# Optimization experiments

Measured on AMD Instinct MI355X. Metric: run time of the kernel, lower is better.

The kernel has to match this reference:

```python
import jax, jax.numpy as jnp
import numpy as np

B, L, D = 2, 2048, 1024
H, HD = 16, 64
MAX_LEN = 4096


def rotate_half(t):
    t1, t2 = jnp.split(t, 2, axis=-1)
    return jnp.concatenate([-t2, t1], axis=-1)


def setup_inputs() -> dict:
    key = jax.random.key(0)
    ks = jax.random.split(key, 6)
    # rope tables computed the standard way (cos/sin of position*inv_freq)
    inv_freq = 1.0 / (10000.0 ** (np.arange(0, HD, 2, dtype=np.float32) / HD))
    pos = np.arange(MAX_LEN, dtype=np.float32)
    freqs = np.einsum('l,f->lf', pos, inv_freq)          # [MAX_LEN, HD/2]
    emb = np.concatenate([freqs, freqs], axis=-1)        # [MAX_LEN, HD]
    return {
        'x': jax.random.normal(ks[0], (B, L, D), dtype=jnp.float32),
        'rope_cos': jnp.asarray(np.cos(emb)),
        'rope_sin': jnp.asarray(np.sin(emb)),
        'W_qkv': jax.random.normal(ks[1], (D, 3 * H * HD), dtype=jnp.float32) * (D ** -0.5),
        'W_out': jax.random.normal(ks[2], (H * HD, D), dtype=jnp.float32) * ((H * HD) ** -0.5),
        'b_out': jnp.zeros((D,), dtype=jnp.float32),
    }


def reference(x, rope_cos, rope_sin, W_qkv, W_out, b_out):
    Bb, Ll, Dd = x.shape
    qkv = jnp.einsum('bld,de->ble', x, W_qkv)            # fused QKV projection
    q, k, v = jnp.split(qkv, 3, axis=-1)
    # [B, h, L, d]
    q = q.reshape(Bb, Ll, H, HD).transpose(0, 2, 1, 3)
    k = k.reshape(Bb, Ll, H, HD).transpose(0, 2, 1, 3)
    v = v.reshape(Bb, Ll, H, HD).transpose(0, 2, 1, 3)
    cos = rope_cos[:Ll][None, None, :, :]                # [1,1,L,d]
    sin = rope_sin[:Ll][None, None, :, :]
    q = q * cos + rotate_half(q) * sin
    k = k * cos + rotate_half(k) * sin
    # causal scaled dot-product attention
    scale = HD ** -0.5
    scores = jnp.einsum('bhqd,bhkd->bhqk', q, k) * scale
    causal = jnp.tril(jnp.ones((Ll, Ll), dtype=bool))
    scores = jnp.where(causal[None, None], scores, jnp.finfo(scores.dtype).min)
    attn = jax.nn.softmax(scores, axis=-1)
    out = jnp.einsum('bhqk,bhkd->bhqd', attn, v)
    out = out.transpose(0, 2, 1, 3).reshape(Bb, Ll, H * HD)
    return jnp.einsum('ble,ed->bld', out, W_out) + b_out
```

## Files before the change

### kernel.cpp

```cpp
#include <hip/hip_runtime.h>
#include <math.h>

#define BQ 2
#define LQ 2048
#define DQ 1024
#define HQ 16
#define HDQ 64

typedef __bf16 bf16_t;
typedef bf16_t bf16x4 __attribute__((ext_vector_type(4)));
typedef bf16_t bf16x8 __attribute__((ext_vector_type(8)));
typedef _Float16 f16_t;
typedef f16_t f16x4 __attribute__((ext_vector_type(4)));
typedef f16_t f16x8 __attribute__((ext_vector_type(8)));
typedef float f32x4 __attribute__((ext_vector_type(4)));

__global__ __launch_bounds__(256) void prep_kernel(
    const float* __restrict__ x, const float* __restrict__ Wqkv,
    const float* __restrict__ Wout, const float* __restrict__ cosT,
    const float* __restrict__ sinT,
    bf16_t* __restrict__ xb, bf16_t* __restrict__ Wqkvt,
    bf16_t* __restrict__ Wot, float4* __restrict__ rpk)
{
    __shared__ float t[32][33];
    const int bid = blockIdx.x, tid = threadIdx.x;
    if (bid < 4096) {
        const int i = (bid * 256 + tid) * 4;
        float4 v = *(const float4*)(x + i);
        bf16x4 o;
        o[0] = (bf16_t)v.x; o[1] = (bf16_t)v.y; o[2] = (bf16_t)v.z; o[3] = (bf16_t)v.w;
        *(bf16x4*)(xb + i) = o;
    } else if (bid < 8192) {
        const bool isq = bid < 7168;
        const int b = isq ? bid - 4096 : bid - 7168;
        const int N = isq ? 3072 : 1024;
        const int gx = isq ? 96 : 32;
        const float* in = isq ? Wqkv : Wout;
        bf16_t* out = isq ? Wqkvt : Wot;
        const int k0 = (b / gx) * 32, n0 = (b % gx) * 32;
        const int r = tid >> 3, c4 = (tid & 7) * 4;
        float4 v = *(const float4*)(in + (size_t)(k0 + r) * N + n0 + c4);
        t[r][c4 + 0] = v.x; t[r][c4 + 1] = v.y;
        t[r][c4 + 2] = v.z; t[r][c4 + 3] = v.w;
        __syncthreads();
        bf16x4 o;
        o[0] = (bf16_t)t[c4 + 0][r]; o[1] = (bf16_t)t[c4 + 1][r];
        o[2] = (bf16_t)t[c4 + 2][r]; o[3] = (bf16_t)t[c4 + 3][r];
        *(bf16x4*)(out + (size_t)(n0 + r) * 1024 + k0 + c4) = o;
    } else {
        const int idx = (bid - 8192) * 256 + tid;
        const int i = idx & 15, l = idx >> 4;
        rpk[idx] = make_float4(cosT[l * 64 + i], cosT[l * 64 + 16 + i],
                               sinT[l * 64 + i], sinT[l * 64 + 16 + i]);
    }
}

__global__ __launch_bounds__(256) void qkv_gemm_kernel(
    const bf16_t* __restrict__ A, const bf16_t* __restrict__ Bt,
    bf16_t* __restrict__ qo, bf16_t* __restrict__ ko, f16_t* __restrict__ vo,
    const float4* __restrict__ rpk)
{
    __shared__ __align__(16) bf16_t As[128][64];
    __shared__ __align__(16) bf16_t Bs[128][64];
    const int K = 1024;
    const int tid  = threadIdx.x;
    const int lane = tid & 63;
    const int w    = tid >> 6;
    const int lr   = lane & 15, quad = lane >> 4;
    const int wm   = w & 1, wn = w >> 1;
    const int m0   = blockIdx.y * 128, n0 = blockIdx.x * 128;
    const int srow8 = lane >> 3;
    const int swz   = ((lane & 7) ^ srow8) * 8;
    const int wc    = (lane & 7) * 8;

    f32x4 acc[4][4];
#pragma unroll
    for (int i = 0; i < 4; i++)
#pragma unroll
        for (int j = 0; j < 4; j++)
#pragma unroll
            for (int r = 0; r < 4; r++) acc[i][j][r] = 0.f;

    bf16x8 ar[4], br[4];
#pragma unroll
    for (int j = 0; j < 4; j++) {
        const int rr = (w * 4 + j) * 8 + srow8;
        ar[j] = *(const bf16x8*)(A  + (size_t)(m0 + rr) * K + swz);
        br[j] = *(const bf16x8*)(Bt + (size_t)(n0 + rr) * K + swz);
    }

    for (int k0 = 0; k0 < K; k0 += 64) {
        __syncthreads();
#pragma unroll
        for (int j = 0; j < 4; j++) {
            const int rg = (w * 4 + j) * 8 + srow8;
            *(bf16x8*)(&As[rg][wc]) = ar[j];
            *(bf16x8*)(&Bs[rg][wc]) = br[j];
        }
        __syncthreads();
        if (k0 + 64 < K) {
#pragma unroll
            for (int j = 0; j < 4; j++) {
                const int rr = (w * 4 + j) * 8 + srow8;
                ar[j] = *(const bf16x8*)(A  + (size_t)(m0 + rr) * K + k0 + 64 + swz);
                br[j] = *(const bf16x8*)(Bt + (size_t)(n0 + rr) * K + k0 + 64 + swz);
            }
        }

        bf16x8 af[4][2], bfr[4][2];
#pragma unroll
        for (int t = 0; t < 4; t++)
#pragma unroll
            for (int h = 0; h < 2; h++) {
                const int cA = ((quad + 4 * h) ^ (lr & 7)) * 8;
                af[t][h]  = *(const bf16x8*)(&As[wm * 64 + t * 16 + lr][cA]);
                bfr[t][h] = *(const bf16x8*)(&Bs[wn * 64 + t * 16 + lr][cA]);
            }
#pragma unroll
        for (int h = 0; h < 2; h++)
#pragma unroll
            for (int mt = 0; mt < 4; mt++)
#pragma unroll
                for (int nt = 0; nt < 4; nt++)
                    acc[mt][nt] = __builtin_amdgcn_mfma_f32_16x16x32_bf16(
                        af[mt][h], bfr[nt][h], acc[mt][nt], 0, 0, 0);
    }

    const int which = n0 >> 10;
    const int h = ((n0 & 1023) + wn * 64) >> 6;
    if (which == 2) {
#pragma unroll
        for (int mt = 0; mt < 4; mt++) {
            const int m = m0 + wm * 64 + mt * 16 + quad * 4;
            const int b = m >> 11, l = m & 2047;
            f16_t* p = vo + ((size_t)(b * HQ + h) * HDQ) * LQ + l;
#pragma unroll
            for (int nt = 0; nt < 4; nt++) {
                f16x4 pv;
#pragma unroll
                for (int r = 0; r < 4; r++) pv[r] = (f16_t)acc[mt][nt][r];
                *(f16x4*)(p + (size_t)(nt * 16 + lr) * LQ) = pv;
            }
        }
    } else {
        bf16_t* dst = which ? ko : qo;
        const float qs = which ? 1.0f : 0.18033688011f;
#pragma unroll
        for (int mt = 0; mt < 4; mt++)
#pragma unroll
            for (int r = 0; r < 4; r++) {
                const int m = m0 + wm * 64 + mt * 16 + quad * 4 + r;
                const int b = m >> 11, l = m & 2047;
                const float4 rp = rpk[l * 16 + lr];
                const float a0 = acc[mt][0][r], a1 = acc[mt][1][r];
                const float a2 = acc[mt][2][r], a3 = acc[mt][3][r];
                bf16_t* p = dst + ((size_t)(b * HQ + h) * LQ + l) * HDQ;
                p[lr]      = (bf16_t)((a0 * rp.x - a2 * rp.z) * qs);
                p[16 + lr] = (bf16_t)((a1 * rp.y - a3 * rp.w) * qs);
                p[32 + lr] = (bf16_t)((a2 * rp.x + a0 * rp.z) * qs);
                p[48 + lr] = (bf16_t)((a3 * rp.y + a1 * rp.w) * qs);
            }
    }
}

__global__ __launch_bounds__(256) void out_gemm_kernel(
    const bf16_t* __restrict__ A, const bf16_t* __restrict__ Bt,
    float* __restrict__ fo, const float* __restrict__ bias)
{
    __shared__ __align__(16) bf16_t As[64][64];
    __shared__ __align__(16) bf16_t Bs[128][64];
    const int K = 1024, N = 1024;
    const int tid  = threadIdx.x;
    const int lane = tid & 63;
    const int w    = tid >> 6;
    const int lr   = lane & 15, quad = lane >> 4;
    const int m0   = blockIdx.y * 64, n0 = blockIdx.x * 128;
    const int srow8 = lane >> 3;
    const int swz   = ((lane & 7) ^ srow8) * 8;
    const int wc    = (lane & 7) * 8;

    f32x4 acc[4][2];
#pragma unroll
    for (int i = 0; i < 4; i++)
#pragma unroll
        for (int j = 0; j < 2; j++)
#pragma unroll
            for (int r = 0; r < 4; r++) acc[i][j][r] = 0.f;

    bf16x8 ar[2], br[4];
#pragma unroll
    for (int j = 0; j < 2; j++)
        ar[j] = *(const bf16x8*)(A + (size_t)(m0 + (w * 2 + j) * 8 + srow8) * K + swz);
#pragma unroll
    for (int j = 0; j < 4; j++)
        br[j] = *(const bf16x8*)(Bt + (size_t)(n0 + (w * 4 + j) * 8 + srow8) * K + swz);

    for (int k0 = 0; k0 < K; k0 += 64) {
        __syncthreads();
#pragma unroll
        for (int j = 0; j < 2; j++)
            *(bf16x8*)(&As[(w * 2 + j) * 8 + srow8][wc]) = ar[j];
#pragma unroll
        for (int j = 0; j < 4; j++)
            *(bf16x8*)(&Bs[(w * 4 + j) * 8 + srow8][wc]) = br[j];
        __syncthreads();
        if (k0 + 64 < K) {
#pragma unroll
            for (int j = 0; j < 2; j++)
                ar[j] = *(const bf16x8*)(A + (size_t)(m0 + (w * 2 + j) * 8 + srow8) * K
                                          + k0 + 64 + swz);
#pragma unroll
            for (int j = 0; j < 4; j++)
                br[j] = *(const bf16x8*)(Bt + (size_t)(n0 + (w * 4 + j) * 8 + srow8) * K
                                          + k0 + 64 + swz);
        }

        bf16x8 af[4][2], bfr[2][2];
#pragma unroll
        for (int h = 0; h < 2; h++) {
            const int cA = ((quad + 4 * h) ^ (lr & 7)) * 8;
#pragma unroll
            for (int t = 0; t < 4; t++)
                af[t][h] = *(const bf16x8*)(&As[t * 16 + lr][cA]);
#pragma unroll
            for (int t = 0; t < 2; t++)
                bfr[t][h] = *(const bf16x8*)(&Bs[w * 32 + t * 16 + lr][cA]);
        }
#pragma unroll
        for (int h = 0; h < 2; h++)
#pragma unroll
            for (int mt = 0; mt < 4; mt++)
#pragma unroll
                for (int nt = 0; nt < 2; nt++)
                    acc[mt][nt] = __builtin_amdgcn_mfma_f32_16x16x32_bf16(
                        af[mt][h], bfr[nt][h], acc[mt][nt], 0, 0, 0);
    }

#pragma unroll
    for (int nt = 0; nt < 2; nt++) {
        const int n = n0 + w * 32 + nt * 16 + lr;
        const float bj = bias[n];
#pragma unroll
        for (int mt = 0; mt < 4; mt++)
#pragma unroll
            for (int r = 0; r < 4; r++) {
                const int m = m0 + mt * 16 + quad * 4 + r;
                fo[(size_t)m * N + n] = acc[mt][nt][r] + bj;
            }
    }
}

__global__ __launch_bounds__(256) void attn_kernel6(
    const bf16_t* __restrict__ qb, const bf16_t* __restrict__ kb,
    const f16_t* __restrict__ vtb, bf16_t* __restrict__ ob)
{
    __shared__ __align__(16) bf16_t Kb[2][64][64];
    __shared__ __align__(16) f16_t  Vs[2][64][72];

    const int tid  = threadIdx.x;
    const int lane = tid & 63;
    const int w    = tid >> 6;
    const int quad = lane >> 4;
    const int lr   = lane & 15;
    const int bh   = blockIdx.x;
    const int qt   = 31 - blockIdx.y;

    const bf16_t* Kh = kb  + (size_t)bh * LQ * HDQ;
    const f16_t*  Vh = vtb + (size_t)bh * HDQ * LQ;

    const int r0 = tid >> 3, c0 = (tid & 7) * 8;
    const int r1 = r0 + 32;
    const int ksw = ((tid & 7) ^ (r0 & 7)) * 8;

    f16x4 ones;
#pragma unroll
    for (int j = 0; j < 4; j++) ones[j] = (f16_t)1.0f;

    const int qrow = qt * 64 + w * 16 + lr;
    const bf16_t* qp = qb + ((size_t)bh * LQ + qrow) * HDQ;
    const bf16x8 qa0 = *(const bf16x8*)(qp + quad * 8);
    const bf16x8 qa1 = *(const bf16x8*)(qp + 32 + quad * 8);

    bf16x8 kp0 = *(const bf16x8*)(Kh + (size_t)r0 * HDQ + c0);
    bf16x8 kp1 = *(const bf16x8*)(Kh + (size_t)r1 * HDQ + c0);
    f16x8  vp0 = *(const f16x8*)(Vh + (size_t)r0 * LQ + c0);
    f16x8  vp1 = *(const f16x8*)(Vh + (size_t)r1 * LQ + c0);

    f32x4 Oacc[4], lacc;
#pragma unroll
    for (int d = 0; d < 4; d++)
#pragma unroll
        for (int r = 0; r < 4; r++) Oacc[d][r] = 0.f;
#pragma unroll
    for (int r = 0; r < 4; r++) lacc[r] = 0.f;

    for (int kt = 0; kt <= qt; kt++) {
        const int buf = kt & 1;
        *(bf16x8*)(&Kb[buf][r0][ksw]) = kp0;
        *(bf16x8*)(&Kb[buf][r1][ksw]) = kp1;
        *(f16x8*)(&Vs[buf][r0][c0]) = vp0;
        *(f16x8*)(&Vs[buf][r1][c0]) = vp1;
        __syncthreads();
        if (kt < qt) {
            const bf16_t* kn = Kh + (size_t)(kt + 1) * 64 * HDQ;
            kp0 = *(const bf16x8*)(kn + (size_t)r0 * HDQ + c0);
            kp1 = *(const bf16x8*)(kn + (size_t)r1 * HDQ + c0);
            vp0 = *(const f16x8*)(Vh + (size_t)r0 * LQ + (kt + 1) * 64 + c0);
            vp1 = *(const f16x8*)(Vh + (size_t)r1 * LQ + (kt + 1) * 64 + c0);
        }

        f32x4 s[4];
#pragma unroll
        for (int nt = 0; nt < 4; nt++) {
            const int rsw = lr & 7;
            const bf16x8 kf0 = *(const bf16x8*)(&Kb[buf][nt * 16 + lr][(quad ^ rsw) * 8]);
            const bf16x8 kf1 = *(const bf16x8*)(&Kb[buf][nt * 16 + lr][((quad + 4) ^ rsw) * 8]);
            f32x4 z = {0.f, 0.f, 0.f, 0.f};
            z = __builtin_amdgcn_mfma_f32_16x16x32_bf16(kf0, qa0, z, 0, 0, 0);
            z = __builtin_amdgcn_mfma_f32_16x16x32_bf16(kf1, qa1, z, 0, 0, 0);
            s[nt] = z;
        }
        if (kt == qt) {
#pragma unroll
            for (int nt = 0; nt < 4; nt++)
#pragma unroll
                for (int r = 0; r < 4; r++)
                    if (nt * 16 + quad * 4 + r > w * 16 + lr) s[nt][r] = -INFINITY;
        }
        f16x4 pa[4];
#pragma unroll
        for (int nt = 0; nt < 4; nt++)
#pragma unroll
            for (int r = 0; r < 4; r++)
                pa[nt][r] = (f16_t)__builtin_amdgcn_exp2f(s[nt][r]);

#pragma unroll
        for (int d = 0; d < 4; d++)
#pragma unroll
            for (int nt = 0; nt < 4; nt++) {
                const f16x4 vf = *(const f16x4*)(&Vs[buf][d * 16 + lr][nt * 16 + quad * 4]);
                Oacc[d] = __builtin_amdgcn_mfma_f32_16x16x16f16(pa[nt], vf, Oacc[d], 0, 0, 0);
            }
#pragma unroll
        for (int nt = 0; nt < 4; nt++)
            lacc = __builtin_amdgcn_mfma_f32_16x16x16f16(pa[nt], ones, lacc, 0, 0, 0);
    }

    const int b = bh >> 4, h = bh & 15;
#pragma unroll
    for (int r = 0; r < 4; r++) {
        const float inv = 1.0f / lacc[r];
        const int q = qt * 64 + w * 16 + quad * 4 + r;
        bf16_t* op = ob + ((size_t)(b * LQ + q)) * 1024 + h * 64;
#pragma unroll
        for (int d = 0; d < 4; d++)
            op[d * 16 + lr] = (bf16_t)(Oacc[d][r] * inv);
    }
}

extern "C" void kernel_launch(void* const* d_in, const int* in_sizes, int n_in,
                              void* d_out, int out_size, void* d_ws, size_t ws_size,
                              hipStream_t stream) {
    const float* x        = (const float*)d_in[0];
    const float* rope_cos = (const float*)d_in[1];
    const float* rope_sin = (const float*)d_in[2];
    const float* W_qkv    = (const float*)d_in[3];
    const float* W_out    = (const float*)d_in[4];
    const float* b_out    = (const float*)d_in[5];
    float* out = (float*)d_out;

    char* wsb = (char*)d_ws;
    bf16_t* xb    = (bf16_t*)(wsb);
    bf16_t* qbf   = (bf16_t*)(wsb + ((size_t)8  << 20));
    bf16_t* kbf   = (bf16_t*)(wsb + ((size_t)16 << 20));
    f16_t*  vth   = (f16_t*) (wsb + ((size_t)24 << 20));
    bf16_t* ob    = (bf16_t*)(wsb + ((size_t)32 << 20));
    bf16_t* Wqkvt = (bf16_t*)(wsb + ((size_t)40 << 20));
    bf16_t* Wot   = (bf16_t*)(wsb + ((size_t)46 << 20));
    float4* rpk   = (float4*)(wsb + ((size_t)48 << 20));

    prep_kernel<<<8320, 256, 0, stream>>>(x, W_qkv, W_out, rope_cos, rope_sin,
                                          xb, Wqkvt, Wot, rpk);

    dim3 g1(3072 / 128, 4096 / 128);
    qkv_gemm_kernel<<<g1, 256, 0, stream>>>(xb, Wqkvt, qbf, kbf, vth, rpk);

    dim3 g2(32, 32);
    attn_kernel6<<<g2, 256, 0, stream>>>(qbf, kbf, vth, ob);

    dim3 g3(1024 / 128, 4096 / 64);
    out_gemm_kernel<<<g3, 256, 0, stream>>>(ob, Wot, out, b_out);
}
```

Baseline: 175.2 us.

## Widen attention blocks to 128 query rows with 8 waves sharing K/V tiles

The attention kernel now launches 512-thread blocks covering 128 query rows (8 waves of 16 rows), halving the grid. Each K/V tile staged in LDS is reused by twice as many waves, and each thread loads a single 8-element chunk per tile instead of two. Waves whose rows lie entirely before a key tile skip its compute but still take part in the barriers, so some waves sit idle on the diagonal tiles. Causal masking now uses absolute positions and applies only to tiles that straddle the diagonal.

```diff
diff --git a/kernel.cpp b/kernel.cpp
--- a/kernel.cpp
+++ b/kernel.cpp
@@ -250,7 +250,7 @@
     }
 }
 
-__global__ __launch_bounds__(256) void attn_kernel6(
+__global__ __launch_bounds__(512) void attn_kernel8(
     const bf16_t* __restrict__ qb, const bf16_t* __restrict__ kb,
     const f16_t* __restrict__ vtb, bf16_t* __restrict__ ob)
 {
@@ -263,28 +263,29 @@
     const int quad = lane >> 4;
     const int lr   = lane & 15;
     const int bh   = blockIdx.x;
-    const int qt   = 31 - blockIdx.y;
+    const int qt2  = 15 - blockIdx.y;
 
     const bf16_t* Kh = kb  + (size_t)bh * LQ * HDQ;
     const f16_t*  Vh = vtb + (size_t)bh * HDQ * LQ;
 
-    const int r0 = tid >> 3, c0 = (tid & 7) * 8;
-    const int r1 = r0 + 32;
+    const int r0  = tid >> 3;
+    const int c0  = (tid & 7) * 8;
     const int ksw = ((tid & 7) ^ (r0 & 7)) * 8;
 
     f16x4 ones;
 #pragma unroll
     for (int j = 0; j < 4; j++) ones[j] = (f16_t)1.0f;
 
-    const int qrow = qt * 64 + w * 16 + lr;
+    const int qbase = qt2 * 128 + w * 16;
+    const int qrow  = qbase + lr;
     const bf16_t* qp = qb + ((size_t)bh * LQ + qrow) * HDQ;
     const bf16x8 qa0 = *(const bf16x8*)(qp + quad * 8);
     const bf16x8 qa1 = *(const bf16x8*)(qp + 32 + quad * 8);
 
-    bf16x8 kp0 = *(const bf16x8*)(Kh + (size_t)r0 * HDQ + c0);
-    bf16x8 kp1 = *(const bf16x8*)(Kh + (size_t)r1 * HDQ + c0);
-    f16x8  vp0 = *(const f16x8*)(Vh + (size_t)r0 * LQ + c0);
-    f16x8  vp1 = *(const f16x8*)(Vh + (size_t)r1 * LQ + c0);
+    const int nkt = 2 * qt2 + 2;
+
+    bf16x8 kp = *(const bf16x8*)(Kh + (size_t)r0 * HDQ + c0);
+    f16x8  vp = *(const f16x8*)(Vh + (size_t)r0 * LQ + c0);
 
     f32x4 Oacc[4], lacc;
 #pragma unroll
@@ -294,63 +295,60 @@
 #pragma unroll
     for (int r = 0; r < 4; r++) lacc[r] = 0.f;
 
-    for (int kt = 0; kt <= qt; kt++) {
+    for (int kt = 0; kt < nkt; kt++) {
         const int buf = kt & 1;
-        *(bf16x8*)(&Kb[buf][r0][ksw]) = kp0;
-        *(bf16x8*)(&Kb[buf][r1][ksw]) = kp1;
-        *(f16x8*)(&Vs[buf][r0][c0]) = vp0;
-        *(f16x8*)(&Vs[buf][r1][c0]) = vp1;
-        __syncthreads();
-        if (kt < qt) {
-            const bf16_t* kn = Kh + (size_t)(kt + 1) * 64 * HDQ;
-            kp0 = *(const bf16x8*)(kn + (size_t)r0 * HDQ + c0);
-            kp1 = *(const bf16x8*)(kn + (size_t)r1 * HDQ + c0);
-            vp0 = *(const f16x8*)(Vh + (size_t)r0 * LQ + (kt + 1) * 64 + c0);
-            vp1 = *(const f16x8*)(Vh + (size_t)r1 * LQ + (kt + 1) * 64 + c0);
-        }
-
-        f32x4 s[4];
-#pragma unroll
-        for (int nt = 0; nt < 4; nt++) {
-            const int rsw = lr & 7;
-            const bf16x8 kf0 = *(const bf16x8*)(&Kb[buf][nt * 16 + lr][(quad ^ rsw) * 8]);
-            const bf16x8 kf1 = *(const bf16x8*)(&Kb[buf][nt * 16 + lr][((quad + 4) ^ rsw) * 8]);
-            f32x4 z = {0.f, 0.f, 0.f, 0.f};
-            z = __builtin_amdgcn_mfma_f32_16x16x32_bf16(kf0, qa0, z, 0, 0, 0);
-            z = __builtin_amdgcn_mfma_f32_16x16x32_bf16(kf1, qa1, z, 0, 0, 0);
-            s[nt] = z;
-        }
-        if (kt == qt) {
+        *(bf16x8*)(&Kb[buf][r0][ksw]) = kp;
+        *(f16x8*)(&Vs[buf][r0][c0]) = vp;
+        __syncthreads();
+        if (kt + 1 < nkt) {
+            kp = *(const bf16x8*)(Kh + (size_t)((kt + 1) * 64 + r0) * HDQ + c0);
+            vp = *(const f16x8*)(Vh + (size_t)r0 * LQ + (kt + 1) * 64 + c0);
+        }
+
+        if (kt * 64 <= qbase + 15) {
+            f32x4 s[4];
+#pragma unroll
+            for (int nt = 0; nt < 4; nt++) {
+                const int rsw = lr & 7;
+                const bf16x8 kf0 = *(const bf16x8*)(&Kb[buf][nt * 16 + lr][(quad ^ rsw) * 8]);
+                const bf16x8 kf1 = *(const bf16x8*)(&Kb[buf][nt * 16 + lr][((quad + 4) ^ rsw) * 8]);
+                f32x4 z = {0.f, 0.f, 0.f, 0.f};
+                z = __builtin_amdgcn_mfma_f32_16x16x32_bf16(kf0, qa0, z, 0, 0, 0);
+                z = __builtin_amdgcn_mfma_f32_16x16x32_bf16(kf1, qa1, z, 0, 0, 0);
+                s[nt] = z;
+            }
+            if (kt * 64 + 63 > qbase) {
+#pragma unroll
+                for (int nt = 0; nt < 4; nt++)
+#pragma unroll
+                    for (int r = 0; r < 4; r++)
+                        if (kt * 64 + nt * 16 + quad * 4 + r > qrow) s[nt][r] = -INFINITY;
+            }
+            f16x4 pa[4];
 #pragma unroll
             for (int nt = 0; nt < 4; nt++)
 #pragma unroll
                 for (int r = 0; r < 4; r++)
-                    if (nt * 16 + quad * 4 + r > w * 16 + lr) s[nt][r] = -INFINITY;
-        }
-        f16x4 pa[4];
-#pragma unroll
-        for (int nt = 0; nt < 4; nt++)
-#pragma unroll
-            for (int r = 0; r < 4; r++)
-                pa[nt][r] = (f16_t)__builtin_amdgcn_exp2f(s[nt][r]);
-
-#pragma unroll
-        for (int d = 0; d < 4; d++)
-#pragma unroll
-            for (int nt = 0; nt < 4; nt++) {
-                const f16x4 vf = *(const f16x4*)(&Vs[buf][d * 16 + lr][nt * 16 + quad * 4]);
-                Oacc[d] = __builtin_amdgcn_mfma_f32_16x16x16f16(pa[nt], vf, Oacc[d], 0, 0, 0);
-            }
-#pragma unroll
-        for (int nt = 0; nt < 4; nt++)
-            lacc = __builtin_amdgcn_mfma_f32_16x16x16f16(pa[nt], ones, lacc, 0, 0, 0);
+                    pa[nt][r] = (f16_t)__builtin_amdgcn_exp2f(s[nt][r]);
+
+#pragma unroll
+            for (int d = 0; d < 4; d++)
+#pragma unroll
+                for (int nt = 0; nt < 4; nt++) {
+                    const f16x4 vf = *(const f16x4*)(&Vs[buf][d * 16 + lr][nt * 16 + quad * 4]);
+                    Oacc[d] = __builtin_amdgcn_mfma_f32_16x16x16f16(pa[nt], vf, Oacc[d], 0, 0, 0);
+                }
+#pragma unroll
+            for (int nt = 0; nt < 4; nt++)
+                lacc = __builtin_amdgcn_mfma_f32_16x16x16f16(pa[nt], ones, lacc, 0, 0, 0);
+        }
     }
 
     const int b = bh >> 4, h = bh & 15;
 #pragma unroll
     for (int r = 0; r < 4; r++) {
         const float inv = 1.0f / lacc[r];
-        const int q = qt * 64 + w * 16 + quad * 4 + r;
+        const int q = qbase + quad * 4 + r;
         bf16_t* op = ob + ((size_t)(b * LQ + q)) * 1024 + h * 64;
 #pragma unroll
         for (int d = 0; d < 4; d++)
@@ -385,8 +383,8 @@
     dim3 g1(3072 / 128, 4096 / 128);
     qkv_gemm_kernel<<<g1, 256, 0, stream>>>(xb, Wqkvt, qbf, kbf, vth, rpk);
 
-    dim3 g2(32, 32);
-    attn_kernel6<<<g2, 256, 0, stream>>>(qbf, kbf, vth, ob);
+    dim3 g2(32, 16);
+    attn_kernel8<<<g2, 512, 0, stream>>>(qbf, kbf, vth, ob);
 
     dim3 g3(1024 / 128, 4096 / 64);
     out_gemm_kernel<<<g3, 256, 0, stream>>>(ob, Wot, out, b_out);
```

Result: slower. 178.7 us (+2.0%).
